# Kernel optimization log

Hardware: AMD Instinct MI355X
Metric: run time of the kernel (lower is better)

Reference implementation:

```python
import jax, jax.numpy as jnp
import numpy as np

D_MODEL = 1024
N_HEADS = 16
HEAD_DIM = D_MODEL // N_HEADS
B, T = 4, 2048


def setup_inputs() -> dict:
    key = jax.random.key(0)
    k_x, k_qkv, k_out = jax.random.split(key, 3)
    x = jax.random.normal(k_x, (B, T, D_MODEL), dtype=jnp.float32)
    # nn.Linear(d, 3d, bias=False): weight [3d, d], y = x @ W.T
    W_qkv = jax.random.normal(k_qkv, (3 * D_MODEL, D_MODEL), dtype=jnp.float32) / np.sqrt(D_MODEL)
    W_out = jax.random.normal(k_out, (D_MODEL, D_MODEL), dtype=jnp.float32) / np.sqrt(D_MODEL)
    return {"x": x, "W_qkv": W_qkv, "W_out": W_out}


def reference(x, W_qkv, W_out):
    Bb, Tt, C = x.shape
    qkv = x @ W_qkv.T                       # [B,T,3C]
    q, k, v = jnp.split(qkv, 3, axis=-1)
    # [B,T,C] -> [B,H,T,hd]
    def heads(t):
        return t.reshape(Bb, Tt, N_HEADS, HEAD_DIM).transpose(0, 2, 1, 3)
    q, k, v = heads(q), heads(k), heads(v)
    scale = 1.0 / np.sqrt(HEAD_DIM).astype(np.float32)
    att = jnp.einsum('bhqd,bhkd->bhqk', q, k) * scale  # [B,H,T,T]
    causal = jnp.tril(jnp.ones((Tt, Tt), dtype=bool))  # True = keep
    att = jnp.where(causal[None, None], att, -jnp.inf)
    att = jax.nn.softmax(att, axis=-1)
    out = jnp.einsum('bhqk,bhkd->bhqd', att, v)        # [B,H,T,hd]
    out = out.transpose(0, 2, 1, 3).reshape(Bb, Tt, C)
    return out @ W_out.T
```

## Files before the change

### kernel.cpp

```cpp
#include <hip/hip_runtime.h>
#include <hip/hip_bf16.h>
#include <math.h>
#include <stdint.h>

#define D_MODEL 1024
#define NH 16
#define HD 64
#define BATCH 4
#define SEQ 2048

typedef unsigned short u16;
typedef __attribute__((ext_vector_type(2))) unsigned short u16x2;
typedef __attribute__((ext_vector_type(4))) unsigned short u16x4;
typedef __attribute__((ext_vector_type(8))) unsigned short u16x8;
typedef __attribute__((ext_vector_type(8))) short short8;
typedef __attribute__((ext_vector_type(4))) float f32x4;

__device__ __forceinline__ u16 f2bf(float f) {
  uint32_t u = __float_as_uint(f);
  uint32_t r = (u + 0x7FFFu + ((u >> 16) & 1u)) >> 16;
  return (u16)r;
}
__device__ __forceinline__ float bf2f(u16 h) {
  return __uint_as_float(((uint32_t)h) << 16);
}

__device__ __forceinline__ void gload_lds16(const void* g, void* l) {
  auto gp = (const __attribute__((address_space(1))) uint32_t*)(uintptr_t)(g);
  auto lp = (__attribute__((address_space(3))) uint32_t*)(uintptr_t)(l);
  __builtin_amdgcn_global_load_lds(gp, lp, 16, 0, 0);
}

__launch_bounds__(256)
__global__ void split_hl(const float* __restrict__ in, u16* __restrict__ hi,
                         u16* __restrict__ lo, int n4) {
  int i = blockIdx.x * blockDim.x + threadIdx.x;
  const int stride = gridDim.x * blockDim.x;
  for (; i < n4; i += stride) {
    float4 v = ((const float4*)in)[i];
    u16x4 h, l4;
    h.x = f2bf(v.x); l4.x = f2bf(v.x - bf2f(h.x));
    h.y = f2bf(v.y); l4.y = f2bf(v.y - bf2f(h.y));
    h.z = f2bf(v.z); l4.z = f2bf(v.z - bf2f(h.z));
    h.w = f2bf(v.w); l4.w = f2bf(v.w - bf2f(h.w));
    ((u16x4*)hi)[i] = h;
    ((u16x4*)lo)[i] = l4;
  }
}

template <int SPLIT>
__launch_bounds__(256)
__global__ void gemm_nt_bf16x3(const u16* __restrict__ Ahi, const u16* __restrict__ Alo,
                               const u16* __restrict__ Bhi, const u16* __restrict__ Blo,
                               float* __restrict__ C, u16* __restrict__ Chi,
                               u16* __restrict__ Clo, int M, int N, int K) {
  __shared__ u16 sAh[128][32];
  __shared__ u16 sAl[128][32];
  __shared__ u16 sBh[128][32];
  __shared__ u16 sBl[128][32];

  const int tid = threadIdx.x;
  const int w = tid >> 6;
  const int l = tid & 63;
  const int bm = blockIdx.y * 128;
  const int bn = blockIdx.x * 128;
  const int wr = (w >> 1) * 64;
  const int wc = (w & 1) * 64;

  const int lr = l >> 2;
  const int lco = (l & 3) << 3;

  const u16* gAh = Ahi + (size_t)bm * K;
  const u16* gAl = Alo + (size_t)bm * K;
  const u16* gBh = Bhi + (size_t)bn * K;
  const u16* gBl = Blo + (size_t)bn * K;

  f32x4 acc[4][4] = {};

  const int fr = l & 15;
  const int fko = (l >> 4) << 3;

  for (int k0 = 0; k0 < K; k0 += 32) {
    __syncthreads();
#pragma unroll
    for (int i = 0; i < 2; ++i) {
      const int bo = (w + 4 * i) << 10;
      const int r = (bo >> 6) + lr;
      const size_t go = (size_t)r * K + k0 + lco;
      gload_lds16(gAh + go, (char*)&sAh[0][0] + bo);
      gload_lds16(gAl + go, (char*)&sAl[0][0] + bo);
      gload_lds16(gBh + go, (char*)&sBh[0][0] + bo);
      gload_lds16(gBl + go, (char*)&sBl[0][0] + bo);
    }
    __syncthreads();

    short8 ah[4], al[4], bh[4], bl[4];
#pragma unroll
    for (int m = 0; m < 4; ++m) {
      ah[m] = *(const short8*)&sAh[wr + m * 16 + fr][fko];
      al[m] = *(const short8*)&sAl[wr + m * 16 + fr][fko];
    }
#pragma unroll
    for (int n = 0; n < 4; ++n) {
      bh[n] = *(const short8*)&sBh[wc + n * 16 + fr][fko];
      bl[n] = *(const short8*)&sBl[wc + n * 16 + fr][fko];
    }
#pragma unroll
    for (int m = 0; m < 4; ++m)
#pragma unroll
      for (int n = 0; n < 4; ++n) {
        acc[m][n] = __builtin_amdgcn_mfma_f32_16x16x32_bf16(ah[m], bh[n], acc[m][n], 0, 0, 0);
        acc[m][n] = __builtin_amdgcn_mfma_f32_16x16x32_bf16(ah[m], bl[n], acc[m][n], 0, 0, 0);
        acc[m][n] = __builtin_amdgcn_mfma_f32_16x16x32_bf16(al[m], bh[n], acc[m][n], 0, 0, 0);
      }
  }

#pragma unroll
  for (int m = 0; m < 4; ++m) {
    const int row0 = bm + wr + m * 16 + ((l >> 4) << 2);
#pragma unroll
    for (int n = 0; n < 4; ++n) {
      const int col = bn + wc + n * 16 + fr;
      f32x4 v = acc[m][n];
      if constexpr (SPLIT) {
#pragma unroll
        for (int j = 0; j < 4; ++j) {
          const size_t idx = (size_t)(row0 + j) * N + col;
          u16 hh = f2bf(v[j]);
          Chi[idx] = hh;
          Clo[idx] = f2bf(v[j] - bf2f(hh));
        }
      } else {
        float* cp = C + (size_t)row0 * N + col;
#pragma unroll
        for (int j = 0; j < 4; ++j) cp[(size_t)j * N] = v[j];
      }
    }
  }
}

struct AttnCtx {
  short8 Qh[2], Ql[2];
  f32x4 acc[4];
  float m_run, l_run;
  int q0w;
};

__device__ __forceinline__ void ctx_init(AttnCtx& C, const u16* __restrict__ qkvh,
                                         const u16* __restrict__ qkvl, size_t base,
                                         int q0w, int g, int q16) {
  C.q0w = q0w;
  const size_t qoff = base + (size_t)(q0w + q16) * (3 * D_MODEL);
#pragma unroll
  for (int dh = 0; dh < 2; ++dh) {
    C.Qh[dh] = *(const short8*)(qkvh + qoff + dh * 32 + g * 8);
    C.Ql[dh] = *(const short8*)(qkvl + qoff + dh * 32 + g * 8);
  }
#pragma unroll
  for (int n = 0; n < 4; ++n) C.acc[n] = f32x4{0.f, 0.f, 0.f, 0.f};
  C.m_run = -1e30f;
  C.l_run = 0.f;
}

__device__ __forceinline__ void process_tile(AttnCtx& C, int j0, int g, int q16,
                                             const char* KhB, const char* KlB,
                                             const char* VhB, const char* VlB,
                                             char* PhB, char* PlB) {
  short8 KAh[2][2], KAl[2][2];
#pragma unroll
  for (int t2 = 0; t2 < 2; ++t2)
#pragma unroll
    for (int dh = 0; dh < 2; ++dh) {
      const int row = 16 * t2 + q16;
      const int off = row * 128 + ((dh * 64 + g * 16) ^ ((q16 & 7) << 4));
      KAh[t2][dh] = *(const short8*)(KhB + off);
      KAl[t2][dh] = *(const short8*)(KlB + off);
    }
  f32x4 S[2] = {};
#pragma unroll
  for (int t2 = 0; t2 < 2; ++t2)
#pragma unroll
    for (int dh = 0; dh < 2; ++dh) {
      S[t2] = __builtin_amdgcn_mfma_f32_16x16x32_bf16(KAh[t2][dh], C.Qh[dh], S[t2], 0, 0, 0);
      S[t2] = __builtin_amdgcn_mfma_f32_16x16x32_bf16(KAh[t2][dh], C.Ql[dh], S[t2], 0, 0, 0);
      S[t2] = __builtin_amdgcn_mfma_f32_16x16x32_bf16(KAl[t2][dh], C.Qh[dh], S[t2], 0, 0, 0);
    }
  const int qg = C.q0w + q16;
  float p[8];
  float mx = -1e30f;
#pragma unroll
  for (int t2 = 0; t2 < 2; ++t2)
#pragma unroll
    for (int j = 0; j < 4; ++j) {
      const int kg = j0 + 16 * t2 + 4 * g + j;
      float s = (kg <= qg) ? S[t2][j] * 0.125f : -1e30f;
      p[t2 * 4 + j] = s;
      mx = fmaxf(mx, s);
    }
  mx = fmaxf(mx, __shfl_xor(mx, 16));
  mx = fmaxf(mx, __shfl_xor(mx, 32));
  const float m_new = fmaxf(C.m_run, mx);
  float sum = 0.f;
#pragma unroll
  for (int i = 0; i < 8; ++i) { p[i] = __expf(p[i] - m_new); sum += p[i]; }
  sum += __shfl_xor(sum, 16);
  sum += __shfl_xor(sum, 32);
  const float alpha = __expf(C.m_run - m_new);
  C.m_run = m_new;
  C.l_run = C.l_run * alpha + sum;
#pragma unroll
  for (int t2 = 0; t2 < 2; ++t2) {
    u16x4 ph, pl;
#pragma unroll
    for (int j = 0; j < 4; ++j) {
      float v = p[t2 * 4 + j];
      ph[j] = f2bf(v);
      pl[j] = f2bf(v - bf2f(ph[j]));
    }
    const int off = q16 * 80 + (16 * t2 + 4 * g) * 2;
    *(u16x4*)(PhB + off) = ph;
    *(u16x4*)(PlB + off) = pl;
  }
  float al4[4];
#pragma unroll
  for (int j = 0; j < 4; ++j) al4[j] = __shfl(alpha, 4 * g + j);
#pragma unroll
  for (int n = 0; n < 4; ++n) {
    f32x4 t = C.acc[n];
    t[0] *= al4[0]; t[1] *= al4[1]; t[2] *= al4[2]; t[3] *= al4[3];
    C.acc[n] = t;
  }
  const short8 PAh = *(const short8*)(PhB + q16 * 80 + g * 16);
  const short8 PAl = *(const short8*)(PlB + q16 * 80 + g * 16);
#pragma unroll
  for (int n = 0; n < 4; ++n) {
    const int off = (16 * n + q16) * 80 + g * 16;
    const short8 VBh = *(const short8*)(VhB + off);
    const short8 VBl = *(const short8*)(VlB + off);
    C.acc[n] = __builtin_amdgcn_mfma_f32_16x16x32_bf16(PAh, VBh, C.acc[n], 0, 0, 0);
    C.acc[n] = __builtin_amdgcn_mfma_f32_16x16x32_bf16(PAh, VBl, C.acc[n], 0, 0, 0);
    C.acc[n] = __builtin_amdgcn_mfma_f32_16x16x32_bf16(PAl, VBh, C.acc[n], 0, 0, 0);
  }
}

__device__ __forceinline__ void ctx_epilogue(const AttnCtx& C, u16* __restrict__ Ohi,
                                             u16* __restrict__ Olo, int b, int h,
                                             int g, int q16) {
  float inv[4];
#pragma unroll
  for (int j = 0; j < 4; ++j) inv[j] = 1.0f / __shfl(C.l_run, 4 * g + j);
#pragma unroll
  for (int n = 0; n < 4; ++n)
#pragma unroll
    for (int j = 0; j < 4; ++j) {
      const size_t idx =
          ((size_t)b * SEQ + C.q0w + 4 * g + j) * D_MODEL + h * HD + n * 16 + q16;
      const float v = C.acc[n][j] * inv[j];
      const u16 hh = f2bf(v);
      Ohi[idx] = hh;
      Olo[idx] = f2bf(v - bf2f(hh));
    }
}

__launch_bounds__(256)
__global__ void attn_mfma(const u16* __restrict__ qkvh, const u16* __restrict__ qkvl,
                          u16* __restrict__ Ohi, u16* __restrict__ Olo) {
  __shared__ u16 Kh[32][64], Kl[32][64];
  __shared__ u16 Vh[64][40], Vl[64][40];
  __shared__ u16 Ph[4][16][40], Pl[4][16][40];

  const int tid = threadIdx.x;
  const int w = tid >> 6, l = tid & 63;
  const int g = l >> 4, q16 = l & 15;
  const int pr = blockIdx.x;
  const int qbA = pr, qbB = 31 - pr;
  const int bh = blockIdx.y;
  const int b = bh >> 4, h = bh & 15;
  const size_t base = (size_t)b * SEQ * (3 * D_MODEL) + h * HD;

  char* KhB = (char*)&Kh[0][0];
  char* KlB = (char*)&Kl[0][0];
  char* VhB = (char*)&Vh[0][0];
  char* VlB = (char*)&Vl[0][0];
  char* PhB = (char*)&Ph[w][0][0];
  char* PlB = (char*)&Pl[w][0][0];

  AttnCtx A, B;
  ctx_init(A, qkvh, qkvl, base, qbA * 64 + w * 16, g, q16);
  ctx_init(B, qkvh, qkvl, base, qbB * 64 + w * 16, g, q16);

  const int sk = tid >> 3, sd0 = (tid & 7) * 8;
  const int vd0 = (tid & 31) * 2, vk0 = (tid >> 5) * 4;
  u16x8 kh_r, kl_r;
  u16x2 vh_r[4], vl_r[4];

  auto loadKV = [&](int j0) {
    const size_t srcK = base + D_MODEL + (size_t)(j0 + sk) * (3 * D_MODEL) + sd0;
    kh_r = *(const u16x8*)(qkvh + srcK);
    kl_r = *(const u16x8*)(qkvl + srcK);
    const size_t srcV = base + 2 * D_MODEL + (size_t)(j0 + vk0) * (3 * D_MODEL) + vd0;
#pragma unroll
    for (int r = 0; r < 4; ++r) {
      vh_r[r] = *(const u16x2*)(qkvh + srcV + (size_t)r * (3 * D_MODEL));
      vl_r[r] = *(const u16x2*)(qkvl + srcV + (size_t)r * (3 * D_MODEL));
    }
  };
  auto writeKV = [&]() {
    const int offK = sk * 128 + ((sd0 * 2) ^ ((sk & 7) << 4));
    *(u16x8*)(KhB + offK) = kh_r;
    *(u16x8*)(KlB + offK) = kl_r;
#pragma unroll
    for (int j = 0; j < 2; ++j) {
      u16x4 th, tl;
      th[0] = vh_r[0][j]; th[1] = vh_r[1][j]; th[2] = vh_r[2][j]; th[3] = vh_r[3][j];
      tl[0] = vl_r[0][j]; tl[1] = vl_r[1][j]; tl[2] = vl_r[2][j]; tl[3] = vl_r[3][j];
      const int off = (vd0 + j) * 80 + vk0 * 2;
      *(u16x4*)(VhB + off) = th;
      *(u16x4*)(VlB + off) = tl;
    }
  };

  const int ktiles = 2 * qbB + 2;
  loadKV(0);
  for (int kt = 0; kt < ktiles; ++kt) {
    const int j0 = kt * 32;
    __syncthreads();
    writeKV();
    __syncthreads();
    if (kt + 1 < ktiles) loadKV((kt + 1) * 32);
    if (j0 <= B.q0w + 15) process_tile(B, j0, g, q16, KhB, KlB, VhB, VlB, PhB, PlB);
    if (j0 <= A.q0w + 15) process_tile(A, j0, g, q16, KhB, KlB, VhB, VlB, PhB, PlB);
  }

  ctx_epilogue(B, Ohi, Olo, b, h, g, q16);
  ctx_epilogue(A, Ohi, Olo, b, h, g, q16);
}

extern "C" void kernel_launch(void* const* d_in, const int* in_sizes, int n_in,
                              void* d_out, int out_size, void* d_ws, size_t ws_size,
                              hipStream_t stream) {
  const float* x    = (const float*)d_in[0];
  const float* Wqkv = (const float*)d_in[1];
  const float* Wout = (const float*)d_in[2];
  float* out = (float*)d_out;

  const int M = BATCH * SEQ;
  const int N1 = 3 * D_MODEL;
  const size_t MB = 1024 * 1024;

  char* ws = (char*)d_ws;
  u16* qkvh = (u16*)(ws);
  u16* qkvl = (u16*)(ws + 48 * MB);
  u16* xhi  = (u16*)(ws + 96 * MB);
  u16* xlo  = (u16*)(ws + 112 * MB);
  u16* whi  = (u16*)(ws + 128 * MB);
  u16* wlo  = (u16*)(ws + 134 * MB);
  u16* ohi  = (u16*)(ws + 140 * MB);
  u16* olo  = (u16*)(ws + 142 * MB);
  u16* ahi  = (u16*)(ws + 96 * MB);
  u16* alo  = (u16*)(ws + 112 * MB);

  split_hl<<<2048, 256, 0, stream>>>(x,    xhi, xlo, M * D_MODEL / 4);
  split_hl<<<2048, 256, 0, stream>>>(Wqkv, whi, wlo, N1 * D_MODEL / 4);
  split_hl<<<1024, 256, 0, stream>>>(Wout, ohi, olo, D_MODEL * D_MODEL / 4);

  gemm_nt_bf16x3<1><<<dim3(N1 / 128, M / 128), 256, 0, stream>>>(
      xhi, xlo, whi, wlo, nullptr, qkvh, qkvl, M, N1, D_MODEL);

  attn_mfma<<<dim3(SEQ / 128, BATCH * NH), 256, 0, stream>>>(qkvh, qkvl, ahi, alo);

  gemm_nt_bf16x3<0><<<dim3(D_MODEL / 128, M / 128), 256, 0, stream>>>(
      ahi, alo, ohi, olo, out, nullptr, nullptr, M, D_MODEL, D_MODEL);
}
```

Before: 533.8 us.

## Process both query contexts per K/V tile jointly and use exp2 softmax

The attention inner loop now processes the two query blocks (A and B) together whenever both are active. K fragments and V fragments are read from LDS once and feed the interleaved MFMA chains of both contexts, and each context gets its own per-wave P buffer. The aim is to cut redundant LDS reads and expose more independent MFMA work for latency hiding, at the cost of higher register pressure. Softmax also switches to exp2f with the scale prefolded by log2(e), and the float-to-bf16 conversion uses the HIP intrinsic.

```diff
diff --git a/kernel.cpp b/kernel.cpp
--- a/kernel.cpp
+++ b/kernel.cpp
@@ -17,9 +17,10 @@
 typedef __attribute__((ext_vector_type(4))) float f32x4;
 
 __device__ __forceinline__ u16 f2bf(float f) {
-  uint32_t u = __float_as_uint(f);
-  uint32_t r = (u + 0x7FFFu + ((u >> 16) & 1u)) >> 16;
-  return (u16)r;
+  __hip_bfloat16 h = __float2bfloat16(f);
+  u16 u;
+  __builtin_memcpy(&u, &h, sizeof(u));
+  return u;
 }
 __device__ __forceinline__ float bf2f(u16 h) {
   return __uint_as_float(((uint32_t)h) << 16);
@@ -139,6 +140,8 @@
   }
 }
 
+#define SC2 0.18033688011112042f
+
 struct AttnCtx {
   short8 Qh[2], Ql[2];
   f32x4 acc[4];
@@ -162,29 +165,8 @@
   C.l_run = 0.f;
 }
 
-__device__ __forceinline__ void process_tile(AttnCtx& C, int j0, int g, int q16,
-                                             const char* KhB, const char* KlB,
-                                             const char* VhB, const char* VlB,
-                                             char* PhB, char* PlB) {
-  short8 KAh[2][2], KAl[2][2];
-#pragma unroll
-  for (int t2 = 0; t2 < 2; ++t2)
-#pragma unroll
-    for (int dh = 0; dh < 2; ++dh) {
-      const int row = 16 * t2 + q16;
-      const int off = row * 128 + ((dh * 64 + g * 16) ^ ((q16 & 7) << 4));
-      KAh[t2][dh] = *(const short8*)(KhB + off);
-      KAl[t2][dh] = *(const short8*)(KlB + off);
-    }
-  f32x4 S[2] = {};
-#pragma unroll
-  for (int t2 = 0; t2 < 2; ++t2)
-#pragma unroll
-    for (int dh = 0; dh < 2; ++dh) {
-      S[t2] = __builtin_amdgcn_mfma_f32_16x16x32_bf16(KAh[t2][dh], C.Qh[dh], S[t2], 0, 0, 0);
-      S[t2] = __builtin_amdgcn_mfma_f32_16x16x32_bf16(KAh[t2][dh], C.Ql[dh], S[t2], 0, 0, 0);
-      S[t2] = __builtin_amdgcn_mfma_f32_16x16x32_bf16(KAl[t2][dh], C.Qh[dh], S[t2], 0, 0, 0);
-    }
+__device__ __forceinline__ void softmax_store(AttnCtx& C, const f32x4 S[2], int j0,
+                                              int g, int q16, char* PhS, char* PlS) {
   const int qg = C.q0w + q16;
   float p[8];
   float mx = -1e30f;
@@ -193,7 +175,7 @@
 #pragma unroll
     for (int j = 0; j < 4; ++j) {
       const int kg = j0 + 16 * t2 + 4 * g + j;
-      float s = (kg <= qg) ? S[t2][j] * 0.125f : -1e30f;
+      float s = (kg <= qg) ? S[t2][j] * SC2 : -1e30f;
       p[t2 * 4 + j] = s;
       mx = fmaxf(mx, s);
     }
@@ -202,10 +184,10 @@
   const float m_new = fmaxf(C.m_run, mx);
   float sum = 0.f;
 #pragma unroll
-  for (int i = 0; i < 8; ++i) { p[i] = __expf(p[i] - m_new); sum += p[i]; }
+  for (int i = 0; i < 8; ++i) { p[i] = exp2f(p[i] - m_new); sum += p[i]; }
   sum += __shfl_xor(sum, 16);
   sum += __shfl_xor(sum, 32);
-  const float alpha = __expf(C.m_run - m_new);
+  const float alpha = exp2f(C.m_run - m_new);
   C.m_run = m_new;
   C.l_run = C.l_run * alpha + sum;
 #pragma unroll
@@ -218,8 +200,8 @@
       pl[j] = f2bf(v - bf2f(ph[j]));
     }
     const int off = q16 * 80 + (16 * t2 + 4 * g) * 2;
-    *(u16x4*)(PhB + off) = ph;
-    *(u16x4*)(PlB + off) = pl;
+    *(u16x4*)(PhS + off) = ph;
+    *(u16x4*)(PlS + off) = pl;
   }
   float al4[4];
 #pragma unroll
@@ -230,16 +212,84 @@
     t[0] *= al4[0]; t[1] *= al4[1]; t[2] *= al4[2]; t[3] *= al4[3];
     C.acc[n] = t;
   }
-  const short8 PAh = *(const short8*)(PhB + q16 * 80 + g * 16);
-  const short8 PAl = *(const short8*)(PlB + q16 * 80 + g * 16);
+}
+
+__device__ __forceinline__ void process_pair(AttnCtx& A, AttnCtx& B, int j0, int g,
+                                             int q16, const char* KhB, const char* KlB,
+                                             const char* VhB, const char* VlB,
+                                             char* PhW, char* PlW) {
+  f32x4 SB[2] = {}, SA[2] = {};
+#pragma unroll
+  for (int t2 = 0; t2 < 2; ++t2) {
+    short8 KAh[2], KAl[2];
+#pragma unroll
+    for (int dh = 0; dh < 2; ++dh) {
+      const int off = (16 * t2 + q16) * 128 + ((dh * 64 + g * 16) ^ ((q16 & 7) << 4));
+      KAh[dh] = *(const short8*)(KhB + off);
+      KAl[dh] = *(const short8*)(KlB + off);
+    }
+#pragma unroll
+    for (int dh = 0; dh < 2; ++dh) {
+      SB[t2] = __builtin_amdgcn_mfma_f32_16x16x32_bf16(KAh[dh], B.Qh[dh], SB[t2], 0, 0, 0);
+      SB[t2] = __builtin_amdgcn_mfma_f32_16x16x32_bf16(KAh[dh], B.Ql[dh], SB[t2], 0, 0, 0);
+      SB[t2] = __builtin_amdgcn_mfma_f32_16x16x32_bf16(KAl[dh], B.Qh[dh], SB[t2], 0, 0, 0);
+      SA[t2] = __builtin_amdgcn_mfma_f32_16x16x32_bf16(KAh[dh], A.Qh[dh], SA[t2], 0, 0, 0);
+      SA[t2] = __builtin_amdgcn_mfma_f32_16x16x32_bf16(KAh[dh], A.Ql[dh], SA[t2], 0, 0, 0);
+      SA[t2] = __builtin_amdgcn_mfma_f32_16x16x32_bf16(KAl[dh], A.Qh[dh], SA[t2], 0, 0, 0);
+    }
+  }
+  softmax_store(B, SB, j0, g, q16, PhW, PlW);
+  softmax_store(A, SA, j0, g, q16, PhW + 1280, PlW + 1280);
+  const short8 PBh = *(const short8*)(PhW + q16 * 80 + g * 16);
+  const short8 PBl = *(const short8*)(PlW + q16 * 80 + g * 16);
+  const short8 PAh = *(const short8*)(PhW + 1280 + q16 * 80 + g * 16);
+  const short8 PAl = *(const short8*)(PlW + 1280 + q16 * 80 + g * 16);
 #pragma unroll
   for (int n = 0; n < 4; ++n) {
     const int off = (16 * n + q16) * 80 + g * 16;
     const short8 VBh = *(const short8*)(VhB + off);
     const short8 VBl = *(const short8*)(VlB + off);
-    C.acc[n] = __builtin_amdgcn_mfma_f32_16x16x32_bf16(PAh, VBh, C.acc[n], 0, 0, 0);
-    C.acc[n] = __builtin_amdgcn_mfma_f32_16x16x32_bf16(PAh, VBl, C.acc[n], 0, 0, 0);
-    C.acc[n] = __builtin_amdgcn_mfma_f32_16x16x32_bf16(PAl, VBh, C.acc[n], 0, 0, 0);
+    B.acc[n] = __builtin_amdgcn_mfma_f32_16x16x32_bf16(PBh, VBh, B.acc[n], 0, 0, 0);
+    B.acc[n] = __builtin_amdgcn_mfma_f32_16x16x32_bf16(PBh, VBl, B.acc[n], 0, 0, 0);
+    B.acc[n] = __builtin_amdgcn_mfma_f32_16x16x32_bf16(PBl, VBh, B.acc[n], 0, 0, 0);
+    A.acc[n] = __builtin_amdgcn_mfma_f32_16x16x32_bf16(PAh, VBh, A.acc[n], 0, 0, 0);
+    A.acc[n] = __builtin_amdgcn_mfma_f32_16x16x32_bf16(PAh, VBl, A.acc[n], 0, 0, 0);
+    A.acc[n] = __builtin_amdgcn_mfma_f32_16x16x32_bf16(PAl, VBh, A.acc[n], 0, 0, 0);
+  }
+}
+
+__device__ __forceinline__ void process_single(AttnCtx& B, int j0, int g, int q16,
+                                               const char* KhB, const char* KlB,
+                                               const char* VhB, const char* VlB,
+                                               char* PhW, char* PlW) {
+  f32x4 SB[2] = {};
+#pragma unroll
+  for (int t2 = 0; t2 < 2; ++t2) {
+    short8 KAh[2], KAl[2];
+#pragma unroll
+    for (int dh = 0; dh < 2; ++dh) {
+      const int off = (16 * t2 + q16) * 128 + ((dh * 64 + g * 16) ^ ((q16 & 7) << 4));
+      KAh[dh] = *(const short8*)(KhB + off);
+      KAl[dh] = *(const short8*)(KlB + off);
+    }
+#pragma unroll
+    for (int dh = 0; dh < 2; ++dh) {
+      SB[t2] = __builtin_amdgcn_mfma_f32_16x16x32_bf16(KAh[dh], B.Qh[dh], SB[t2], 0, 0, 0);
+      SB[t2] = __builtin_amdgcn_mfma_f32_16x16x32_bf16(KAh[dh], B.Ql[dh], SB[t2], 0, 0, 0);
+      SB[t2] = __builtin_amdgcn_mfma_f32_16x16x32_bf16(KAl[dh], B.Qh[dh], SB[t2], 0, 0, 0);
+    }
+  }
+  softmax_store(B, SB, j0, g, q16, PhW, PlW);
+  const short8 PBh = *(const short8*)(PhW + q16 * 80 + g * 16);
+  const short8 PBl = *(const short8*)(PlW + q16 * 80 + g * 16);
+#pragma unroll
+  for (int n = 0; n < 4; ++n) {
+    const int off = (16 * n + q16) * 80 + g * 16;
+    const short8 VBh = *(const short8*)(VhB + off);
+    const short8 VBl = *(const short8*)(VlB + off);
+    B.acc[n] = __builtin_amdgcn_mfma_f32_16x16x32_bf16(PBh, VBh, B.acc[n], 0, 0, 0);
+    B.acc[n] = __builtin_amdgcn_mfma_f32_16x16x32_bf16(PBh, VBl, B.acc[n], 0, 0, 0);
+    B.acc[n] = __builtin_amdgcn_mfma_f32_16x16x32_bf16(PBl, VBh, B.acc[n], 0, 0, 0);
   }
 }
 
@@ -267,7 +317,7 @@
                           u16* __restrict__ Ohi, u16* __restrict__ Olo) {
   __shared__ u16 Kh[32][64], Kl[32][64];
   __shared__ u16 Vh[64][40], Vl[64][40];
-  __shared__ u16 Ph[4][16][40], Pl[4][16][40];
+  __shared__ u16 Ph[4][2][16][40], Pl[4][2][16][40];
 
   const int tid = threadIdx.x;
   const int w = tid >> 6, l = tid & 63;
@@ -282,8 +332,8 @@
   char* KlB = (char*)&Kl[0][0];
   char* VhB = (char*)&Vh[0][0];
   char* VlB = (char*)&Vl[0][0];
-  char* PhB = (char*)&Ph[w][0][0];
-  char* PlB = (char*)&Pl[w][0][0];
+  char* PhW = (char*)&Ph[w][0][0][0];
+  char* PlW = (char*)&Pl[w][0][0][0];
 
   AttnCtx A, B;
   ctx_init(A, qkvh, qkvl, base, qbA * 64 + w * 16, g, q16);
@@ -328,8 +378,10 @@
     writeKV();
     __syncthreads();
     if (kt + 1 < ktiles) loadKV((kt + 1) * 32);
-    if (j0 <= B.q0w + 15) process_tile(B, j0, g, q16, KhB, KlB, VhB, VlB, PhB, PlB);
-    if (j0 <= A.q0w + 15) process_tile(A, j0, g, q16, KhB, KlB, VhB, VlB, PhB, PlB);
+    const bool actA = j0 <= A.q0w + 15;
+    const bool actB = j0 <= B.q0w + 15;
+    if (actA)      process_pair(A, B, j0, g, q16, KhB, KlB, VhB, VlB, PhW, PlW);
+    else if (actB) process_single(B, j0, g, q16, KhB, KlB, VhB, VlB, PhW, PlW);
   }
 
   ctx_epilogue(B, Ohi, Olo, b, h, g, q16);
```

Result: slower. 566.7 us (+6.2%).

## Process four query blocks per attention workgroup sharing K/V tiles

Applied to the files above, without the earlier changes.

Each attention block now handles four balanced query blocks (pr, 15-pr, 16+pr, 31-pr) instead of two, so each K/V tile staged in shared memory and each K fragment read is reused across four contexts. The grid shrinks to 8 blocks per head, and only half the threads load V, using wider vector loads. Softmax switches to exp2f with a pre-folded log2e scale, f2bf uses the library bf16 conversion, and launch bounds request two blocks per CU. The cost is higher register pressure from four accumulator contexts and fewer blocks in flight, which could hurt occupancy.

```diff
diff --git a/kernel.cpp b/kernel.cpp
--- a/kernel.cpp
+++ b/kernel.cpp
@@ -17,9 +17,10 @@
 typedef __attribute__((ext_vector_type(4))) float f32x4;
 
 __device__ __forceinline__ u16 f2bf(float f) {
-  uint32_t u = __float_as_uint(f);
-  uint32_t r = (u + 0x7FFFu + ((u >> 16) & 1u)) >> 16;
-  return (u16)r;
+  __hip_bfloat16 h = __float2bfloat16(f);
+  u16 u;
+  __builtin_memcpy(&u, &h, sizeof(u));
+  return u;
 }
 __device__ __forceinline__ float bf2f(u16 h) {
   return __uint_as_float(((uint32_t)h) << 16);
@@ -139,6 +140,8 @@
   }
 }
 
+#define SC2 0.18033688011112042f
+
 struct AttnCtx {
   short8 Qh[2], Ql[2];
   f32x4 acc[4];
@@ -162,20 +165,58 @@
   C.l_run = 0.f;
 }
 
-__device__ __forceinline__ void process_tile(AttnCtx& C, int j0, int g, int q16,
-                                             const char* KhB, const char* KlB,
-                                             const char* VhB, const char* VlB,
-                                             char* PhB, char* PlB) {
-  short8 KAh[2][2], KAl[2][2];
+__device__ __forceinline__ void softmax_store(AttnCtx& C, const f32x4 S[2], int j0,
+                                              int g, int q16, char* PhS, char* PlS) {
+  const int qg = C.q0w + q16;
+  float p[8];
+  float mx = -1e30f;
 #pragma unroll
   for (int t2 = 0; t2 < 2; ++t2)
 #pragma unroll
-    for (int dh = 0; dh < 2; ++dh) {
-      const int row = 16 * t2 + q16;
-      const int off = row * 128 + ((dh * 64 + g * 16) ^ ((q16 & 7) << 4));
-      KAh[t2][dh] = *(const short8*)(KhB + off);
-      KAl[t2][dh] = *(const short8*)(KlB + off);
-    }
+    for (int j = 0; j < 4; ++j) {
+      const int kg = j0 + 16 * t2 + 4 * g + j;
+      float s = (kg <= qg) ? S[t2][j] * SC2 : -1e30f;
+      p[t2 * 4 + j] = s;
+      mx = fmaxf(mx, s);
+    }
+  mx = fmaxf(mx, __shfl_xor(mx, 16));
+  mx = fmaxf(mx, __shfl_xor(mx, 32));
+  const float m_new = fmaxf(C.m_run, mx);
+  float sum = 0.f;
+#pragma unroll
+  for (int i = 0; i < 8; ++i) { p[i] = exp2f(p[i] - m_new); sum += p[i]; }
+  sum += __shfl_xor(sum, 16);
+  sum += __shfl_xor(sum, 32);
+  const float alpha = exp2f(C.m_run - m_new);
+  C.m_run = m_new;
+  C.l_run = C.l_run * alpha + sum;
+#pragma unroll
+  for (int t2 = 0; t2 < 2; ++t2) {
+    u16x4 ph, pl;
+#pragma unroll
+    for (int j = 0; j < 4; ++j) {
+      float v = p[t2 * 4 + j];
+      ph[j] = f2bf(v);
+      pl[j] = f2bf(v - bf2f(ph[j]));
+    }
+    const int off = q16 * 80 + (16 * t2 + 4 * g) * 2;
+    *(u16x4*)(PhS + off) = ph;
+    *(u16x4*)(PlS + off) = pl;
+  }
+  float al4[4];
+#pragma unroll
+  for (int j = 0; j < 4; ++j) al4[j] = __shfl(alpha, 4 * g + j);
+#pragma unroll
+  for (int n = 0; n < 4; ++n) {
+    f32x4 t = C.acc[n];
+    t[0] *= al4[0]; t[1] *= al4[1]; t[2] *= al4[2]; t[3] *= al4[3];
+    C.acc[n] = t;
+  }
+}
+
+__device__ __forceinline__ void qk_softmax(AttnCtx& C, const short8 (&KAh)[2][2],
+                                           const short8 (&KAl)[2][2], int j0, int g,
+                                           int q16, char* PhS, char* PlS) {
   f32x4 S[2] = {};
 #pragma unroll
   for (int t2 = 0; t2 < 2; ++t2)
@@ -185,62 +226,7 @@
       S[t2] = __builtin_amdgcn_mfma_f32_16x16x32_bf16(KAh[t2][dh], C.Ql[dh], S[t2], 0, 0, 0);
       S[t2] = __builtin_amdgcn_mfma_f32_16x16x32_bf16(KAl[t2][dh], C.Qh[dh], S[t2], 0, 0, 0);
     }
-  const int qg = C.q0w + q16;
-  float p[8];
-  float mx = -1e30f;
-#pragma unroll
-  for (int t2 = 0; t2 < 2; ++t2)
-#pragma unroll
-    for (int j = 0; j < 4; ++j) {
-      const int kg = j0 + 16 * t2 + 4 * g + j;
-      float s = (kg <= qg) ? S[t2][j] * 0.125f : -1e30f;
-      p[t2 * 4 + j] = s;
-      mx = fmaxf(mx, s);
-    }
-  mx = fmaxf(mx, __shfl_xor(mx, 16));
-  mx = fmaxf(mx, __shfl_xor(mx, 32));
-  const float m_new = fmaxf(C.m_run, mx);
-  float sum = 0.f;
-#pragma unroll
-  for (int i = 0; i < 8; ++i) { p[i] = __expf(p[i] - m_new); sum += p[i]; }
-  sum += __shfl_xor(sum, 16);
-  sum += __shfl_xor(sum, 32);
-  const float alpha = __expf(C.m_run - m_new);
-  C.m_run = m_new;
-  C.l_run = C.l_run * alpha + sum;
-#pragma unroll
-  for (int t2 = 0; t2 < 2; ++t2) {
-    u16x4 ph, pl;
-#pragma unroll
-    for (int j = 0; j < 4; ++j) {
-      float v = p[t2 * 4 + j];
-      ph[j] = f2bf(v);
-      pl[j] = f2bf(v - bf2f(ph[j]));
-    }
-    const int off = q16 * 80 + (16 * t2 + 4 * g) * 2;
-    *(u16x4*)(PhB + off) = ph;
-    *(u16x4*)(PlB + off) = pl;
-  }
-  float al4[4];
-#pragma unroll
-  for (int j = 0; j < 4; ++j) al4[j] = __shfl(alpha, 4 * g + j);
-#pragma unroll
-  for (int n = 0; n < 4; ++n) {
-    f32x4 t = C.acc[n];
-    t[0] *= al4[0]; t[1] *= al4[1]; t[2] *= al4[2]; t[3] *= al4[3];
-    C.acc[n] = t;
-  }
-  const short8 PAh = *(const short8*)(PhB + q16 * 80 + g * 16);
-  const short8 PAl = *(const short8*)(PlB + q16 * 80 + g * 16);
-#pragma unroll
-  for (int n = 0; n < 4; ++n) {
-    const int off = (16 * n + q16) * 80 + g * 16;
-    const short8 VBh = *(const short8*)(VhB + off);
-    const short8 VBl = *(const short8*)(VlB + off);
-    C.acc[n] = __builtin_amdgcn_mfma_f32_16x16x32_bf16(PAh, VBh, C.acc[n], 0, 0, 0);
-    C.acc[n] = __builtin_amdgcn_mfma_f32_16x16x32_bf16(PAh, VBl, C.acc[n], 0, 0, 0);
-    C.acc[n] = __builtin_amdgcn_mfma_f32_16x16x32_bf16(PAl, VBh, C.acc[n], 0, 0, 0);
-  }
+  softmax_store(C, S, j0, g, q16, PhS, PlS);
 }
 
 __device__ __forceinline__ void ctx_epilogue(const AttnCtx& C, u16* __restrict__ Ohi,
@@ -262,18 +248,17 @@
     }
 }
 
-__launch_bounds__(256)
+__launch_bounds__(256, 2)
 __global__ void attn_mfma(const u16* __restrict__ qkvh, const u16* __restrict__ qkvl,
                           u16* __restrict__ Ohi, u16* __restrict__ Olo) {
   __shared__ u16 Kh[32][64], Kl[32][64];
   __shared__ u16 Vh[64][40], Vl[64][40];
-  __shared__ u16 Ph[4][16][40], Pl[4][16][40];
+  __shared__ u16 Ph[4][4][16][40], Pl[4][4][16][40];
 
   const int tid = threadIdx.x;
   const int w = tid >> 6, l = tid & 63;
   const int g = l >> 4, q16 = l & 15;
   const int pr = blockIdx.x;
-  const int qbA = pr, qbB = 31 - pr;
   const int bh = blockIdx.y;
   const int b = bh >> 4, h = bh & 15;
   const size_t base = (size_t)b * SEQ * (3 * D_MODEL) + h * HD;
@@ -282,45 +267,51 @@
   char* KlB = (char*)&Kl[0][0];
   char* VhB = (char*)&Vh[0][0];
   char* VlB = (char*)&Vl[0][0];
-  char* PhB = (char*)&Ph[w][0][0];
-  char* PlB = (char*)&Pl[w][0][0];
-
-  AttnCtx A, B;
-  ctx_init(A, qkvh, qkvl, base, qbA * 64 + w * 16, g, q16);
-  ctx_init(B, qkvh, qkvl, base, qbB * 64 + w * 16, g, q16);
+  char* PhW = (char*)&Ph[w][0][0][0];
+  char* PlW = (char*)&Pl[w][0][0][0];
+
+  AttnCtx D, C, B, A;
+  ctx_init(D, qkvh, qkvl, base, (31 - pr) * 64 + w * 16, g, q16);
+  ctx_init(C, qkvh, qkvl, base, (16 + pr) * 64 + w * 16, g, q16);
+  ctx_init(B, qkvh, qkvl, base, (15 - pr) * 64 + w * 16, g, q16);
+  ctx_init(A, qkvh, qkvl, base, pr * 64 + w * 16, g, q16);
 
   const int sk = tid >> 3, sd0 = (tid & 7) * 8;
-  const int vd0 = (tid & 31) * 2, vk0 = (tid >> 5) * 4;
+  const int vd0 = (tid >> 3) * 4, vk0 = (tid & 7) * 4;
   u16x8 kh_r, kl_r;
-  u16x2 vh_r[4], vl_r[4];
+  u16x4 vh_r[4], vl_r[4];
 
   auto loadKV = [&](int j0) {
     const size_t srcK = base + D_MODEL + (size_t)(j0 + sk) * (3 * D_MODEL) + sd0;
     kh_r = *(const u16x8*)(qkvh + srcK);
     kl_r = *(const u16x8*)(qkvl + srcK);
-    const size_t srcV = base + 2 * D_MODEL + (size_t)(j0 + vk0) * (3 * D_MODEL) + vd0;
-#pragma unroll
-    for (int r = 0; r < 4; ++r) {
-      vh_r[r] = *(const u16x2*)(qkvh + srcV + (size_t)r * (3 * D_MODEL));
-      vl_r[r] = *(const u16x2*)(qkvl + srcV + (size_t)r * (3 * D_MODEL));
+    if (tid < 128) {
+      const size_t srcV = base + 2 * D_MODEL + (size_t)(j0 + vk0) * (3 * D_MODEL) + vd0;
+#pragma unroll
+      for (int r = 0; r < 4; ++r) {
+        vh_r[r] = *(const u16x4*)(qkvh + srcV + (size_t)r * (3 * D_MODEL));
+        vl_r[r] = *(const u16x4*)(qkvl + srcV + (size_t)r * (3 * D_MODEL));
+      }
     }
   };
   auto writeKV = [&]() {
     const int offK = sk * 128 + ((sd0 * 2) ^ ((sk & 7) << 4));
     *(u16x8*)(KhB + offK) = kh_r;
     *(u16x8*)(KlB + offK) = kl_r;
-#pragma unroll
-    for (int j = 0; j < 2; ++j) {
-      u16x4 th, tl;
-      th[0] = vh_r[0][j]; th[1] = vh_r[1][j]; th[2] = vh_r[2][j]; th[3] = vh_r[3][j];
-      tl[0] = vl_r[0][j]; tl[1] = vl_r[1][j]; tl[2] = vl_r[2][j]; tl[3] = vl_r[3][j];
-      const int off = (vd0 + j) * 80 + vk0 * 2;
-      *(u16x4*)(VhB + off) = th;
-      *(u16x4*)(VlB + off) = tl;
+    if (tid < 128) {
+#pragma unroll
+      for (int j = 0; j < 4; ++j) {
+        u16x4 th, tl;
+        th[0] = vh_r[0][j]; th[1] = vh_r[1][j]; th[2] = vh_r[2][j]; th[3] = vh_r[3][j];
+        tl[0] = vl_r[0][j]; tl[1] = vl_r[1][j]; tl[2] = vl_r[2][j]; tl[3] = vl_r[3][j];
+        const int off = (vd0 + j) * 80 + vk0 * 2;
+        *(u16x4*)(VhB + off) = th;
+        *(u16x4*)(VlB + off) = tl;
+      }
     }
   };
 
-  const int ktiles = 2 * qbB + 2;
+  const int ktiles = 2 * (31 - pr) + 2;
   loadKV(0);
   for (int kt = 0; kt < ktiles; ++kt) {
     const int j0 = kt * 32;
@@ -328,10 +319,62 @@
     writeKV();
     __syncthreads();
     if (kt + 1 < ktiles) loadKV((kt + 1) * 32);
-    if (j0 <= B.q0w + 15) process_tile(B, j0, g, q16, KhB, KlB, VhB, VlB, PhB, PlB);
-    if (j0 <= A.q0w + 15) process_tile(A, j0, g, q16, KhB, KlB, VhB, VlB, PhB, PlB);
-  }
-
+
+    const bool actC = j0 <= C.q0w + 15;
+    const bool actB = j0 <= B.q0w + 15;
+    const bool actA = j0 <= A.q0w + 15;
+
+    short8 KAh[2][2], KAl[2][2];
+#pragma unroll
+    for (int t2 = 0; t2 < 2; ++t2)
+#pragma unroll
+      for (int dh = 0; dh < 2; ++dh) {
+        const int off = (16 * t2 + q16) * 128 + ((dh * 64 + g * 16) ^ ((q16 & 7) << 4));
+        KAh[t2][dh] = *(const short8*)(KhB + off);
+        KAl[t2][dh] = *(const short8*)(KlB + off);
+      }
+
+    qk_softmax(D, KAh, KAl, j0, g, q16, PhW, PlW);
+    if (actC) qk_softmax(C, KAh, KAl, j0, g, q16, PhW + 1280, PlW + 1280);
+    if (actB) qk_softmax(B, KAh, KAl, j0, g, q16, PhW + 2560, PlW + 2560);
+    if (actA) qk_softmax(A, KAh, KAl, j0, g, q16, PhW + 3840, PlW + 3840);
+
+    const int pf = q16 * 80 + g * 16;
+    short8 PDh = *(const short8*)(PhW + pf);
+    short8 PDl = *(const short8*)(PlW + pf);
+    short8 PCh, PCl, PBh, PBl, PAh, PAl;
+    if (actC) { PCh = *(const short8*)(PhW + 1280 + pf); PCl = *(const short8*)(PlW + 1280 + pf); }
+    if (actB) { PBh = *(const short8*)(PhW + 2560 + pf); PBl = *(const short8*)(PlW + 2560 + pf); }
+    if (actA) { PAh = *(const short8*)(PhW + 3840 + pf); PAl = *(const short8*)(PlW + 3840 + pf); }
+
+#pragma unroll
+    for (int n = 0; n < 4; ++n) {
+      const int off = (16 * n + q16) * 80 + g * 16;
+      const short8 VBh = *(const short8*)(VhB + off);
+      const short8 VBl = *(const short8*)(VlB + off);
+      D.acc[n] = __builtin_amdgcn_mfma_f32_16x16x32_bf16(PDh, VBh, D.acc[n], 0, 0, 0);
+      D.acc[n] = __builtin_amdgcn_mfma_f32_16x16x32_bf16(PDh, VBl, D.acc[n], 0, 0, 0);
+      D.acc[n] = __builtin_amdgcn_mfma_f32_16x16x32_bf16(PDl, VBh, D.acc[n], 0, 0, 0);
+      if (actC) {
+        C.acc[n] = __builtin_amdgcn_mfma_f32_16x16x32_bf16(PCh, VBh, C.acc[n], 0, 0, 0);
+        C.acc[n] = __builtin_amdgcn_mfma_f32_16x16x32_bf16(PCh, VBl, C.acc[n], 0, 0, 0);
+        C.acc[n] = __builtin_amdgcn_mfma_f32_16x16x32_bf16(PCl, VBh, C.acc[n], 0, 0, 0);
+      }
+      if (actB) {
+        B.acc[n] = __builtin_amdgcn_mfma_f32_16x16x32_bf16(PBh, VBh, B.acc[n], 0, 0, 0);
+        B.acc[n] = __builtin_amdgcn_mfma_f32_16x16x32_bf16(PBh, VBl, B.acc[n], 0, 0, 0);
+        B.acc[n] = __builtin_amdgcn_mfma_f32_16x16x32_bf16(PBl, VBh, B.acc[n], 0, 0, 0);
+      }
+      if (actA) {
+        A.acc[n] = __builtin_amdgcn_mfma_f32_16x16x32_bf16(PAh, VBh, A.acc[n], 0, 0, 0);
+        A.acc[n] = __builtin_amdgcn_mfma_f32_16x16x32_bf16(PAh, VBl, A.acc[n], 0, 0, 0);
+        A.acc[n] = __builtin_amdgcn_mfma_f32_16x16x32_bf16(PAl, VBh, A.acc[n], 0, 0, 0);
+      }
+    }
+  }
+
+  ctx_epilogue(D, Ohi, Olo, b, h, g, q16);
+  ctx_epilogue(C, Ohi, Olo, b, h, g, q16);
   ctx_epilogue(B, Ohi, Olo, b, h, g, q16);
   ctx_epilogue(A, Ohi, Olo, b, h, g, q16);
 }
@@ -367,7 +410,7 @@
   gemm_nt_bf16x3<1><<<dim3(N1 / 128, M / 128), 256, 0, stream>>>(
       xhi, xlo, whi, wlo, nullptr, qkvh, qkvl, M, N1, D_MODEL);
 
-  attn_mfma<<<dim3(SEQ / 128, BATCH * NH), 256, 0, stream>>>(qkvh, qkvl, ahi, alo);
+  attn_mfma<<<dim3(8, BATCH * NH), 256, 0, stream>>>(qkvh, qkvl, ahi, alo);
 
   gemm_nt_bf16x3<0><<<dim3(D_MODEL / 128, M / 128), 256, 0, stream>>>(
       ahi, alo, ohi, olo, out, nullptr, nullptr, M, D_MODEL, D_MODEL);
```

New measurement: 546.7 us. +2.4%, slower.
